# Kernel tuning notes

Measured on AMD Instinct MI355X. Metric: run time of the kernel, lower is better.

Reference implementation:

```python
import jax, jax.numpy as jnp
import numpy as np

HEADS = 4
KDIM = 512
HALF = KDIM // 2
KNN = 16
NKEYS = 512
INPUT_DIM = 1024
VDIM = 512
B, T = 2, 1024


def setup_inputs() -> dict:
    key = jax.random.key(0)
    ks = jax.random.split(key, 5)
    bound_k = 1.0 / np.sqrt(KDIM)
    x = jax.random.normal(ks[0], (B, T, INPUT_DIM), dtype=jnp.float32)
    Wq = jax.random.normal(ks[1], (HEADS * KDIM, INPUT_DIM), dtype=jnp.float32) * (1.0 / np.sqrt(INPUT_DIM))
    bq = jnp.zeros((HEADS * KDIM,), dtype=jnp.float32)
    keys = jax.random.uniform(ks[2], (2 * HEADS * NKEYS, HALF), dtype=jnp.float32, minval=-bound_k, maxval=bound_k)
    values = jax.random.normal(ks[3], (NKEYS * NKEYS, VDIM), dtype=jnp.float32) * (VDIM ** -0.5)
    return {"x": x, "Wq": Wq, "bq": bq, "keys": keys, "values": values}


def reference(x, Wq, bq, keys, values):
    Bb, Tt, C = x.shape
    bs = Bb * Tt
    x_flat = x.reshape(bs, C)
    # query projection -> (bs, heads, k_dim)
    q = (x_flat @ Wq.T + bq).reshape(bs, HEADS, KDIM)
    q1, q2 = q[..., :HALF], q[..., HALF:]
    kk = keys.reshape(HEADS, 2, NKEYS, HALF)
    k1, k2 = kk[:, 0], kk[:, 1]
    # subspace scores: (bs, heads, n_keys)
    s1 = jnp.einsum('blh,lkh->blk', q1, k1)
    s2 = jnp.einsum('blh,lkh->blk', q2, k2)
    s1, i1 = jax.lax.top_k(s1, KNN)
    s2, i2 = jax.lax.top_k(s2, KNN)
    # cartesian merge -> (bs, heads, knn*knn)
    all_s = (s1[:, :, :, None] + s2[:, :, None, :]).reshape(bs, HEADS, KNN * KNN)
    all_i = (i1[:, :, :, None] * NKEYS + i2[:, :, None, :]).reshape(bs, HEADS, KNN * KNN)
    s, best = jax.lax.top_k(all_s, KNN)
    idx = jnp.take_along_axis(all_i, best, axis=2)  # (bs, heads, knn)
    # softmax per (token, head) over knn, in fp32 (matches torch F.softmax on (bs*heads, knn))
    w = jax.nn.softmax(s.astype(jnp.float32), axis=-1)
    idx_f = idx.reshape(bs, HEADS * KNN)
    w_f = w.reshape(bs, HEADS * KNN)
    # embedding_bag mode='sum' with per-sample weights
    out = jnp.einsum('bk,bkd->bd', w_f, values[idx_f].astype(jnp.float32))
    return out.reshape(Bb, Tt, VDIM).astype(x.dtype)
```

## Files before the change

### kernel.cpp

```cpp
#include <hip/hip_runtime.h>

typedef __attribute__((ext_vector_type(8))) _Float16 half8;
typedef __attribute__((ext_vector_type(4)))  float   floatx4;
typedef __attribute__((ext_vector_type(2)))  float   floatx2;
typedef unsigned short ushort;

__device__ __forceinline__ void gl_lds16(const void* g, void* lds) {
    __builtin_amdgcn_global_load_lds(
        (const __attribute__((address_space(1))) unsigned int*)g,
        (__attribute__((address_space(3))) unsigned int*)lds,
        16, 0, 0);
}

__global__ void split2_kernel(const float* __restrict__ src,
                              _Float16* __restrict__ ph,
                              _Float16* __restrict__ pl, int n8) {
    int i = blockIdx.x * 256 + threadIdx.x;
    if (i >= n8) return;
    const float* s = src + (size_t)i * 8;
    floatx4 a = *(const floatx4*)s;
    floatx4 b = *(const floatx4*)(s + 4);
    float x[8];
    #pragma unroll
    for (int j = 0; j < 4; ++j) { x[j] = a[j]; x[j + 4] = b[j]; }
    half8 vh, vl;
    #pragma unroll
    for (int j = 0; j < 8; ++j) {
        _Float16 h = (_Float16)x[j];
        _Float16 l = (_Float16)((x[j] - (float)h) * 4096.0f);
        vh[j] = h; vl[j] = l;
    }
    *(half8*)(ph + (size_t)i * 8) = vh;
    *(half8*)(pl + (size_t)i * 8) = vl;
}

#define BM 128
#define BN 64
#define BK 32

template<int MODE>
__global__ __launch_bounds__(256) void gemm2_kernel(
    const _Float16* __restrict__ Ah, const _Float16* __restrict__ Al, int lda,
    const _Float16* __restrict__ Bh, const _Float16* __restrict__ Bl, int ldb,
    int K, const float* __restrict__ bias,
    float* __restrict__ C1, float* __restrict__ C2,
    _Float16* __restrict__ Qh, _Float16* __restrict__ Ql, int ldc)
{
    __shared__ _Float16 As[2][2][BM][BK];
    __shared__ _Float16 Bs[2][2][BN][BK];

    const int tid  = threadIdx.x;
    const int lane = tid & 63;
    const int w    = tid >> 6;
    const int wr   = w >> 1;
    const int wc   = w & 1;

    const size_t aRow = (size_t)blockIdx.y * BM;
    const size_t bRow = (size_t)blockIdx.x * BN;
    const _Float16 *Ah_p = Ah, *Al_p = Al, *Bh_p = Bh, *Bl_p = Bl;
    float* Cout = C1;
    if (MODE == 1) {
        int z = blockIdx.z;
        int h = z >> 1, c = z & 1;
        size_t aoff = (size_t)h * 512 + (size_t)c * 256;
        Ah_p += aoff; Al_p += aoff;
        size_t boff = (size_t)z * 512 * (size_t)ldb;
        Bh_p += boff; Bl_p += boff;
        Cout = (c ? C2 : C1) + (size_t)h * 512;
    }

    const int rr = lane >> 2;
    const int jj = (lane & 3) ^ ((lane >> 3) & 3);
    const size_t aStage = (aRow + rr) * (size_t)lda + jj * 8;
    const size_t bStage = (bRow + rr) * (size_t)ldb + jj * 8;

    const int rchunk = (lane >> 4) ^ ((lane >> 1) & 3);
    const int arow0  = wr * 64 + (lane & 15);
    const int brow0  = wc * 32 + (lane & 15);

#define STAGE(buf, ktoff)                                                      \
    {                                                                          \
        _Float16* As0s = &As[buf][0][0][0];                                    \
        _Float16* Bs0s = &Bs[buf][0][0][0];                                    \
        for (int i = w; i < 24; i += 4) {                                      \
            if (i < 16) {                                                      \
                int p = i >> 3, g = i & 7;                                     \
                const _Float16* base = p ? Al_p : Ah_p;                        \
                gl_lds16(base + aStage + (size_t)(g * 16) * lda + (ktoff),     \
                         (void*)(As0s + p * (BM * BK) + g * 16 * BK));         \
            } else {                                                           \
                int p = (i >> 2) & 1, g = i & 3;                               \
                const _Float16* base = p ? Bl_p : Bh_p;                        \
                gl_lds16(base + bStage + (size_t)(g * 16) * ldb + (ktoff),     \
                         (void*)(Bs0s + p * (BN * BK) + g * 16 * BK));         \
            }                                                                  \
        }                                                                      \
    }

    floatx4 acc0[4][2], acc1[4][2];
    #pragma unroll
    for (int m = 0; m < 4; ++m)
        #pragma unroll
        for (int n = 0; n < 2; ++n) { acc0[m][n] = (floatx4)0.0f; acc1[m][n] = (floatx4)0.0f; }

    const int NT = K / BK;

    STAGE(0, 0);
    __syncthreads();

    int cur = 0;
    for (int t = 0; t < NT; ++t) {
        if (t + 1 < NT) STAGE(cur ^ 1, (t + 1) * BK);

        const _Float16* As0 = &As[cur][0][0][0];
        const _Float16* Bs0 = &Bs[cur][0][0][0];
        half8 a_h[4], a_l[4], b_h[2], b_l[2];
        #pragma unroll
        for (int m = 0; m < 4; ++m) {
            int off = (arow0 + m * 16) * BK + rchunk * 8;
            a_h[m] = *(const half8*)(As0 + off);
            a_l[m] = *(const half8*)(As0 + BM * BK + off);
        }
        #pragma unroll
        for (int n = 0; n < 2; ++n) {
            int off = (brow0 + n * 16) * BK + rchunk * 8;
            b_h[n] = *(const half8*)(Bs0 + off);
            b_l[n] = *(const half8*)(Bs0 + BN * BK + off);
        }
        #pragma unroll
        for (int m = 0; m < 4; ++m)
            #pragma unroll
            for (int n = 0; n < 2; ++n) {
                acc0[m][n] = __builtin_amdgcn_mfma_f32_16x16x32_f16(a_h[m], b_h[n], acc0[m][n], 0, 0, 0);
                acc1[m][n] = __builtin_amdgcn_mfma_f32_16x16x32_f16(a_h[m], b_l[n], acc1[m][n], 0, 0, 0);
                acc1[m][n] = __builtin_amdgcn_mfma_f32_16x16x32_f16(a_l[m], b_h[n], acc1[m][n], 0, 0, 0);
            }

        __syncthreads();
        cur ^= 1;
    }
#undef STAGE

    #pragma unroll
    for (int m = 0; m < 4; ++m)
        #pragma unroll
        for (int n = 0; n < 2; ++n)
            #pragma unroll
            for (int r = 0; r < 4; ++r) {
                size_t row = aRow + wr * 64 + m * 16 + (lane >> 4) * 4 + r;
                size_t col = bRow + wc * 32 + n * 16 + (lane & 15);
                float v = acc0[m][n][r] + acc1[m][n][r] * (1.0f / 4096.0f);
                if (MODE == 0) {
                    v += bias[col];
                    _Float16 h = (_Float16)v;
                    _Float16 l = (_Float16)((v - (float)h) * 4096.0f);
                    Qh[row * ldc + col] = h;
                    Ql[row * ldc + col] = l;
                } else {
                    Cout[row * ldc + col] = v;
                }
            }
}

template<int L>
__device__ __forceinline__ void wave_topk16_reg(float (&v)[L], int lane,
                                                float (&selv)[16], int (&seli)[16]) {
    #pragma unroll
    for (int s = 0; s < 16; ++s) {
        float bv = v[0]; int bj = 0;
        #pragma unroll
        for (int j = 1; j < L; ++j) if (v[j] > bv) { bv = v[j]; bj = j; }
        int bi = lane * L + bj;
        #pragma unroll
        for (int off = 32; off > 0; off >>= 1) {
            float ov = __shfl_xor(bv, off, 64);
            int   oi = __shfl_xor(bi, off, 64);
            if (ov > bv || (ov == bv && oi < bi)) { bv = ov; bi = oi; }
        }
        selv[s] = bv; seli[s] = bi;
        int lj = bi - lane * L;
        #pragma unroll
        for (int j = 0; j < L; ++j) if (j == lj) v[j] = -3.4e38f;
    }
}

__global__ __launch_bounds__(256) void topk_gather_kernel(
    const float* __restrict__ s1, const float* __restrict__ s2,
    const float* __restrict__ values, float* __restrict__ out)
{
    __shared__ float sa[4][16];  __shared__ int ia_sh[4][16];
    __shared__ float sb[4][16];  __shared__ int ib_sh[4][16];
    __shared__ float wgt[4][16]; __shared__ int vidx[4][16];

    const int t = blockIdx.x, tid = threadIdx.x;
    const int h = tid >> 6, lane = tid & 63;

    const float* r1 = s1 + ((size_t)t * 4 + h) * 512;
    const float* r2 = s2 + ((size_t)t * 4 + h) * 512;
    float v1[8], v2[8];
    {
        floatx4 a0 = *(const floatx4*)(r1 + lane * 8);
        floatx4 a1 = *(const floatx4*)(r1 + lane * 8 + 4);
        floatx4 b0 = *(const floatx4*)(r2 + lane * 8);
        floatx4 b1 = *(const floatx4*)(r2 + lane * 8 + 4);
        #pragma unroll
        for (int j = 0; j < 4; ++j) { v1[j] = a0[j]; v1[j + 4] = a1[j]; v2[j] = b0[j]; v2[j + 4] = b1[j]; }
    }

    float selv1[16]; int seli1[16];
    wave_topk16_reg<8>(v1, lane, selv1, seli1);
    float selv2[16]; int seli2[16];
    wave_topk16_reg<8>(v2, lane, selv2, seli2);

    if (lane == 0) {
        #pragma unroll
        for (int s = 0; s < 16; ++s) {
            sa[h][s] = selv1[s]; ia_sh[h][s] = seli1[s];
            sb[h][s] = selv2[s]; ib_sh[h][s] = seli2[s];
        }
    }
    __syncthreads();

    float cv[4];
    #pragma unroll
    for (int cc = 0; cc < 4; ++cc) {
        int id = lane * 4 + cc;
        cv[cc] = sa[h][id >> 4] + sb[h][id & 15];
    }
    float fs[16]; int fid[16];
    wave_topk16_reg<4>(cv, lane, fs, fid);

    if (lane == 0) {
        float m = fs[0], sum = 0.f, e[16];
        #pragma unroll
        for (int s = 0; s < 16; ++s) { e[s] = expf(fs[s] - m); sum += e[s]; }
        float inv = 1.f / sum;
        #pragma unroll
        for (int s = 0; s < 16; ++s) {
            int id = fid[s];
            wgt[h][s]  = e[s] * inv;
            vidx[h][s] = ia_sh[h][id >> 4] * 512 + ib_sh[h][id & 15];
        }
    }
    __syncthreads();

    const int col = tid * 2;
    float ax = 0.f, ay = 0.f;
    #pragma unroll 4
    for (int e2 = 0; e2 < 64; ++e2) {
        int hh = e2 >> 4, k = e2 & 15;
        float wv = wgt[hh][k];
        int   id = vidx[hh][k];
        floatx2 v = *(const floatx2*)(values + (size_t)id * 512 + col);
        ax += wv * v[0]; ay += wv * v[1];
    }
    floatx2 o; o[0] = ax; o[1] = ay;
    *(floatx2*)(out + (size_t)t * 512 + col) = o;
}

extern "C" void kernel_launch(void* const* d_in, const int* in_sizes, int n_in,
                              void* d_out, int out_size, void* d_ws, size_t ws_size,
                              hipStream_t stream) {
    (void)in_sizes; (void)n_in; (void)out_size; (void)ws_size;
    const float* x      = (const float*)d_in[0];
    const float* Wq     = (const float*)d_in[1];
    const float* bq     = (const float*)d_in[2];
    const float* keys   = (const float*)d_in[3];
    const float* values = (const float*)d_in[4];
    float* out = (float*)d_out;

    char* ws = (char*)d_ws;
    const size_t MB = 1024 * 1024;
    _Float16* xh = (_Float16*)(ws + 0 * MB);
    _Float16* xl = (_Float16*)(ws + 4 * MB);
    _Float16* wh = (_Float16*)(ws + 8 * MB);
    _Float16* wl = (_Float16*)(ws + 12 * MB);
    _Float16* kh = (_Float16*)(ws + 16 * MB);
    _Float16* kl = (_Float16*)(ws + 18 * MB);
    _Float16* qh = (_Float16*)(ws + 20 * MB);
    _Float16* ql = (_Float16*)(ws + 28 * MB);
    float*    s1 = (float*)(ws + 36 * MB);
    float*    s2 = (float*)(ws + 52 * MB);

    split2_kernel<<<1024, 256, 0, stream>>>(x,    xh, xl, 262144);
    split2_kernel<<<1024, 256, 0, stream>>>(Wq,   wh, wl, 262144);
    split2_kernel<<<512,  256, 0, stream>>>(keys, kh, kl, 131072);

    gemm2_kernel<0><<<dim3(2048 / BN, 2048 / BM, 1), 256, 0, stream>>>(
        xh, xl, 1024, wh, wl, 1024, 1024, bq,
        nullptr, nullptr, qh, ql, 2048);

    gemm2_kernel<1><<<dim3(512 / BN, 2048 / BM, 8), 256, 0, stream>>>(
        qh, ql, 2048, kh, kl, 256, 256, nullptr,
        s1, s2, nullptr, nullptr, 2048);

    topk_gather_kernel<<<2048, 256, 0, stream>>>(s1, s2, values, out);
}
```

Measured before the change: 214.9 us.

## Fuse three split launches into one and shrink GEMM M-tile to 64

Combines the three fp32-to-split-fp16 conversion launches into a single kernel that picks its source by block index, removing two launch overheads. It also halves the GEMM block tile in M (BM 128 to 64), which doubles the grid size and halves the per-wave accumulators and LDS use. The aim is better CU occupancy for the query projection and score GEMMs. The cost is less data reuse per block and more redundant B-tile loads.

```diff
diff --git a/kernel.cpp b/kernel.cpp
--- a/kernel.cpp
+++ b/kernel.cpp
@@ -12,29 +12,35 @@
         16, 0, 0);
 }
 
-__global__ void split2_kernel(const float* __restrict__ src,
-                              _Float16* __restrict__ ph,
-                              _Float16* __restrict__ pl, int n8) {
-    int i = blockIdx.x * 256 + threadIdx.x;
-    if (i >= n8) return;
+__global__ void split_all_kernel(const float* __restrict__ x,
+                                 const float* __restrict__ Wq,
+                                 const float* __restrict__ keys,
+                                 _Float16* __restrict__ xh, _Float16* __restrict__ xl,
+                                 _Float16* __restrict__ wh, _Float16* __restrict__ wl,
+                                 _Float16* __restrict__ kh, _Float16* __restrict__ kl) {
+    int b = blockIdx.x;
+    const float* src; _Float16 *ph, *pl; int i;
+    if (b < 1024)      { src = x;    ph = xh; pl = xl; i = b * 256 + threadIdx.x; }
+    else if (b < 2048) { src = Wq;   ph = wh; pl = wl; i = (b - 1024) * 256 + threadIdx.x; }
+    else               { src = keys; ph = kh; pl = kl; i = (b - 2048) * 256 + threadIdx.x; }
     const float* s = src + (size_t)i * 8;
     floatx4 a = *(const floatx4*)s;
-    floatx4 b = *(const floatx4*)(s + 4);
-    float x[8];
-    #pragma unroll
-    for (int j = 0; j < 4; ++j) { x[j] = a[j]; x[j + 4] = b[j]; }
+    floatx4 bb = *(const floatx4*)(s + 4);
+    float v[8];
+    #pragma unroll
+    for (int j = 0; j < 4; ++j) { v[j] = a[j]; v[j + 4] = bb[j]; }
     half8 vh, vl;
     #pragma unroll
     for (int j = 0; j < 8; ++j) {
-        _Float16 h = (_Float16)x[j];
-        _Float16 l = (_Float16)((x[j] - (float)h) * 4096.0f);
+        _Float16 h = (_Float16)v[j];
+        _Float16 l = (_Float16)((v[j] - (float)h) * 4096.0f);
         vh[j] = h; vl[j] = l;
     }
     *(half8*)(ph + (size_t)i * 8) = vh;
     *(half8*)(pl + (size_t)i * 8) = vl;
 }
 
-#define BM 128
+#define BM 64
 #define BN 64
 #define BK 32
 
@@ -75,21 +81,22 @@
     const size_t bStage = (bRow + rr) * (size_t)ldb + jj * 8;
 
     const int rchunk = (lane >> 4) ^ ((lane >> 1) & 3);
-    const int arow0  = wr * 64 + (lane & 15);
+    const int arow0  = wr * 32 + (lane & 15);
     const int brow0  = wc * 32 + (lane & 15);
 
 #define STAGE(buf, ktoff)                                                      \
     {                                                                          \
         _Float16* As0s = &As[buf][0][0][0];                                    \
         _Float16* Bs0s = &Bs[buf][0][0][0];                                    \
-        for (int i = w; i < 24; i += 4) {                                      \
-            if (i < 16) {                                                      \
-                int p = i >> 3, g = i & 7;                                     \
+        for (int i = w; i < 16; i += 4) {                                      \
+            if (i < 8) {                                                       \
+                int p = i >> 2, g = i & 3;                                     \
                 const _Float16* base = p ? Al_p : Ah_p;                        \
                 gl_lds16(base + aStage + (size_t)(g * 16) * lda + (ktoff),     \
                          (void*)(As0s + p * (BM * BK) + g * 16 * BK));         \
             } else {                                                           \
-                int p = (i >> 2) & 1, g = i & 3;                               \
+                int j = i & 7;                                                 \
+                int p = j >> 2, g = j & 3;                                     \
                 const _Float16* base = p ? Bl_p : Bh_p;                        \
                 gl_lds16(base + bStage + (size_t)(g * 16) * ldb + (ktoff),     \
                          (void*)(Bs0s + p * (BN * BK) + g * 16 * BK));         \
@@ -97,9 +104,9 @@
         }                                                                      \
     }
 
-    floatx4 acc0[4][2], acc1[4][2];
-    #pragma unroll
-    for (int m = 0; m < 4; ++m)
+    floatx4 acc0[2][2], acc1[2][2];
+    #pragma unroll
+    for (int m = 0; m < 2; ++m)
         #pragma unroll
         for (int n = 0; n < 2; ++n) { acc0[m][n] = (floatx4)0.0f; acc1[m][n] = (floatx4)0.0f; }
 
@@ -114,9 +121,9 @@
 
         const _Float16* As0 = &As[cur][0][0][0];
         const _Float16* Bs0 = &Bs[cur][0][0][0];
-        half8 a_h[4], a_l[4], b_h[2], b_l[2];
-        #pragma unroll
-        for (int m = 0; m < 4; ++m) {
+        half8 a_h[2], a_l[2], b_h[2], b_l[2];
+        #pragma unroll
+        for (int m = 0; m < 2; ++m) {
             int off = (arow0 + m * 16) * BK + rchunk * 8;
             a_h[m] = *(const half8*)(As0 + off);
             a_l[m] = *(const half8*)(As0 + BM * BK + off);
@@ -128,7 +135,7 @@
             b_l[n] = *(const half8*)(Bs0 + BN * BK + off);
         }
         #pragma unroll
-        for (int m = 0; m < 4; ++m)
+        for (int m = 0; m < 2; ++m)
             #pragma unroll
             for (int n = 0; n < 2; ++n) {
                 acc0[m][n] = __builtin_amdgcn_mfma_f32_16x16x32_f16(a_h[m], b_h[n], acc0[m][n], 0, 0, 0);
@@ -142,12 +149,12 @@
 #undef STAGE
 
     #pragma unroll
-    for (int m = 0; m < 4; ++m)
+    for (int m = 0; m < 2; ++m)
         #pragma unroll
         for (int n = 0; n < 2; ++n)
             #pragma unroll
             for (int r = 0; r < 4; ++r) {
-                size_t row = aRow + wr * 64 + m * 16 + (lane >> 4) * 4 + r;
+                size_t row = aRow + wr * 32 + m * 16 + (lane >> 4) * 4 + r;
                 size_t col = bRow + wc * 32 + n * 16 + (lane & 15);
                 float v = acc0[m][n][r] + acc1[m][n][r] * (1.0f / 4096.0f);
                 if (MODE == 0) {
@@ -282,9 +289,7 @@
     float*    s1 = (float*)(ws + 36 * MB);
     float*    s2 = (float*)(ws + 52 * MB);
 
-    split2_kernel<<<1024, 256, 0, stream>>>(x,    xh, xl, 262144);
-    split2_kernel<<<1024, 256, 0, stream>>>(Wq,   wh, wl, 262144);
-    split2_kernel<<<512,  256, 0, stream>>>(keys, kh, kl, 131072);
+    split_all_kernel<<<2560, 256, 0, stream>>>(x, Wq, keys, xh, xl, wh, wl, kh, kl);
 
     gemm2_kernel<0><<<dim3(2048 / BN, 2048 / BM, 1), 256, 0, stream>>>(
         xh, xl, 1024, wh, wl, 1024, 1024, bq,
```

Result: faster. 204.6 us (-4.8%).
